# Optimization experiments

Measured on AMD Instinct MI355X. Metric: run time of the kernel, lower is better.

Reference implementation:

```python
import jax, jax.numpy as jnp
import numpy as np

C = 256
RATIO = 8
D = C // RATIO  # 32

def setup_inputs() -> dict:
    key = jax.random.key(0)
    ks = jax.random.split(key, 8)
    B, H, W = 8, 64, 64
    x = jax.random.normal(ks[0], (B, C, H, W), dtype=jnp.float32)
    s = 1.0 / np.sqrt(C)
    wq = jax.random.normal(ks[1], (D, C), dtype=jnp.float32) * s
    bq = jax.random.normal(ks[2], (D,), dtype=jnp.float32) * 0.01
    wk = jax.random.normal(ks[3], (D, C), dtype=jnp.float32) * s
    bk = jax.random.normal(ks[4], (D,), dtype=jnp.float32) * 0.01
    wv = jax.random.normal(ks[5], (C, C), dtype=jnp.float32) * s
    bv = jax.random.normal(ks[6], (C,), dtype=jnp.float32) * 0.01
    gamma = jnp.zeros((1,), dtype=jnp.float32) + 0.5  # nonzero so output depends on attention
    return {"x": x, "wq": wq, "bq": bq, "wk": wk, "bk": bk, "wv": wv, "bv": bv, "gamma": gamma}

def reference(x, wq, bq, wk, bk, wv, bv, gamma):
    B, Cc, Hh, Ww = x.shape
    N = Hh * Ww
    xf = x.reshape(B, Cc, N)                      # b c n
    q = jnp.einsum('dc,bcn->bdn', wq, xf) + bq[None, :, None]   # b d n
    k = jnp.einsum('dc,bcn->bdn', wk, xf) + bk[None, :, None]
    v = jnp.einsum('ec,bcn->ben', wv, xf) + bv[None, :, None]   # b C n
    energy = jnp.einsum('bdn,bdm->bnm', q, k)     # b n m (query n, key m)
    attn = jax.nn.softmax(energy, axis=-1)
    out = jnp.einsum('bcm,bnm->bcn', v, attn)     # out[:, :, n] = sum_m v[:, :, m]*attn[n, m]
    out = gamma[0] * out + xf
    return out.reshape(B, Cc, Hh, Ww)
```

## Files before the change

kernel.cpp:

```cpp
#include <hip/hip_runtime.h>

namespace {

using f4 = __attribute__((ext_vector_type(4))) float;
using s8 = __attribute__((ext_vector_type(8))) short;
using u16x8 = __attribute__((ext_vector_type(8))) unsigned short;

constexpr int kN = 4096;
constexpr int kC = 256;
constexpr int kD = 32;
constexpr int kB = 8;
constexpr int BR = 64;
constexpr int NT = 128;
constexpr int NI = 64;

__device__ __forceinline__ unsigned short f2bf(float x) {
  union { float f; unsigned u; } v{x};
  unsigned r = v.u + 0x7fffu + ((v.u >> 16) & 1u);
  return (unsigned short)(r >> 16);
}
__device__ __forceinline__ float bf2f(unsigned short h) {
  union { unsigned u; float f; } v{((unsigned)h) << 16};
  return v.f;
}
__device__ __forceinline__ void gll16(const void* g, void* l) {
  __builtin_amdgcn_global_load_lds(
      (const __attribute__((address_space(1))) unsigned int*)g,
      (__attribute__((address_space(3))) unsigned int*)l, 16, 0, 0);
}

__global__ void wswz_kernel(const float* __restrict__ wq,
                            const float* __restrict__ wk,
                            const float* __restrict__ wv,
                            unsigned short* __restrict__ wswz) {
  const int mt = blockIdx.x;
  const int t = threadIdx.x;
  const int s = t & 63;
  const int m = s & 15, quad = s >> 4;
  const int kk = t >> 6;
  const float* w;
  int row0;
  if (mt < 2) { w = wq; row0 = mt * 16; }
  else if (mt < 4) { w = wk; row0 = (mt - 2) * 16; }
  else { w = wv; row0 = (mt - 4) * 16; }
  const float* wrow = w + (size_t)(row0 + m) * kC;
#pragma unroll
  for (int e = 0; e < 2; ++e) {
    const int ks = kk * 2 + e;
    const int c0 = ks * 32 + quad * 8;
    u16x8 hi, lo;
#pragma unroll
    for (int j = 0; j < 8; ++j) {
      const float f = wrow[c0 + j];
      const unsigned short h = f2bf(f);
      hi[j] = h;
      lo[j] = f2bf(f - bf2f(h));
    }
    const size_t base = (size_t)mt * 8192 + (size_t)ks * 512 + (size_t)s * 8;
    *(u16x8*)&wswz[base] = hi;
    *(u16x8*)&wswz[base + 4096] = lo;
  }
}

__global__ __launch_bounds__(256, 2) void qkv_kernel(
    const float* __restrict__ x, const float* __restrict__ bq,
    const float* __restrict__ bk, const float* __restrict__ bv,
    const unsigned short* __restrict__ wswz, float* __restrict__ q,
    unsigned short* __restrict__ kswz, unsigned short* __restrict__ vswz) {
  __shared__ __align__(16) unsigned short wlds[2][8192];
  __shared__ __align__(16) unsigned short vls[16 * 72];
  const int t = threadIdx.x, lane = t & 63, wvid = t >> 6;
  const int nn = lane & 15, quad = lane >> 4;
  const int b = blockIdx.y, nb = blockIdx.x * 64;
  const int n_g = nb + wvid * 16 + nn;

  s8 xh[8], xl[8];
#pragma unroll
  for (int ks = 0; ks < 8; ++ks) {
#pragma unroll
    for (int j = 0; j < 8; ++j) {
      const int c = ks * 32 + quad * 8 + j;
      const float f = x[((size_t)(b * kC + c)) * kN + n_g];
      const unsigned short h = f2bf(f);
      xh[ks][j] = (short)h;
      xl[ks][j] = (short)f2bf(f - bf2f(h));
    }
  }

  {
    const unsigned short* gsrc = wswz;
#pragma unroll
    for (int i = 0; i < 4; ++i) {
      const int chunk = i * 4 + wvid;
      gll16(gsrc + chunk * 512 + lane * 8, &wlds[0][chunk * 512 + lane * 8]);
    }
  }

  for (int mt = 0; mt < 20; ++mt) {
    __syncthreads();
    if (mt + 1 < 20) {
      const bool nv = (mt + 1) >= 4;
      const unsigned short* gsrc = wswz + (size_t)(mt + 1) * 8192;
      unsigned short* dst = wlds[(mt + 1) & 1];
      const int niter = nv ? 2 : 4;
      for (int i = 0; i < niter; ++i) {
        const int chunk = i * 4 + wvid;
        gll16(gsrc + chunk * 512 + lane * 8, dst + chunk * 512 + lane * 8);
      }
    }
    const unsigned short* wb = wlds[mt & 1];
    const bool isv = mt >= 4;
    f4 acc = {0.f, 0.f, 0.f, 0.f};
#pragma unroll
    for (int ks = 0; ks < 8; ++ks) {
      const s8 ah = *(const s8*)&wb[ks * 512 + lane * 8];
      acc = __builtin_amdgcn_mfma_f32_16x16x32_bf16(ah, xh[ks], acc, 0, 0, 0);
      acc = __builtin_amdgcn_mfma_f32_16x16x32_bf16(ah, xl[ks], acc, 0, 0, 0);
      if (!isv) {
        const s8 al = *(const s8*)&wb[4096 + ks * 512 + lane * 8];
        acc = __builtin_amdgcn_mfma_f32_16x16x32_bf16(al, xh[ks], acc, 0, 0, 0);
      }
    }
    const int ml = quad * 4;
    if (mt < 2) {
#pragma unroll
      for (int r = 0; r < 4; ++r) {
        const float val = acc[r] + bq[mt * 16 + ml + r];
        q[((size_t)(b * kD + mt * 16 + ml + r)) * kN + n_g] = val;
      }
    } else if (mt < 4) {
      const int nt = n_g >> 5, key5 = n_g & 31;
      const int kb = key5 & 1, cpos = key5 >> 1;
      ushort4 hi, lo;
#pragma unroll
      for (int r = 0; r < 4; ++r) {
        const float val = acc[r] + bk[(mt - 2) * 16 + ml + r];
        const unsigned short h = f2bf(val);
        ((unsigned short*)&hi)[r] = h;
        ((unsigned short*)&lo)[r] = f2bf(val - bf2f(h));
      }
      const int d0 = (mt - 2) * 16 + ml;
      const int qk = d0 >> 3, j0 = d0 & 7;
      const size_t base = ((size_t)((b * NT + nt) * 4 + kb)) * 512 +
                          (size_t)(qk * 16 + cpos) * 8 + j0;
      *(ushort4*)&kswz[base] = hi;
      *(ushort4*)&kswz[base + 1024] = lo;
    } else {
      const int cb = mt - 4;
      const int tk = wvid * 16 + nn;
#pragma unroll
      for (int r = 0; r < 4; ++r) {
        const float val = acc[r] + bv[cb * 16 + ml + r];
        vls[(ml + r) * 72 + tk] = f2bf(val);
      }
      __syncthreads();
      if (t < 128) {
        const int cv = t >> 3, oct = t & 7;
        const u16x8 row = *(const u16x8*)&vls[cv * 72 + oct * 8];
        const int nt = (nb >> 5) + (oct >> 2);
        const int quadv = oct & 3;
        *(u16x8*)&vswz[((size_t)(b * NT + nt)) * 8192 + (size_t)cb * 512 +
                       (size_t)(quadv * 16 + cv) * 8] = row;
      }
    }
  }
}

__global__ __launch_bounds__(256, 2) void attn_kernel(
    const float* __restrict__ q, const unsigned short* __restrict__ kswz,
    const unsigned short* __restrict__ vswz, const float* __restrict__ x,
    const float* __restrict__ gamma, float* __restrict__ out) {
  __shared__ __align__(16) char smem[20480];
  unsigned short* const pA = (unsigned short*)smem;
  unsigned* const pAu = (unsigned*)smem;
  float* const otmp = (float*)smem;

  const int t = threadIdx.x;
  const int lane = t & 63;
  const int wvid = t >> 6;
  const int c = lane & 15;
  const int quad = lane >> 4;
  const int b = blockIdx.y;
  const int nb = blockIdx.x * BR;

  s8 qfh, qfl;
  {
    const int nq = nb + wvid * 16 + c;
#pragma unroll
    for (int j = 0; j < 8; ++j) {
      const int d = quad * 8 + j;
      const float f = q[((size_t)(b * kD + d)) * kN + nq];
      const unsigned short h = f2bf(f);
      qfh[j] = (short)h;
      qfl[j] = (short)f2bf(f - bf2f(h));
    }
  }

  s8 ones;
#pragma unroll
  for (int j = 0; j < 8; ++j) ones[j] = (short)0x3F80;

  f4 O[4][4];
#pragma unroll
  for (int i = 0; i < 4; ++i)
#pragma unroll
    for (int jj = 0; jj < 4; ++jj) O[i][jj] = (f4){0.f, 0.f, 0.f, 0.f};
  f4 Ol[4];
#pragma unroll
  for (int i = 0; i < 4; ++i) Ol[i] = (f4){0.f, 0.f, 0.f, 0.f};

  const s8* gkb = (const s8*)(kswz + ((size_t)(b * NT)) * 2048);
  const s8* gvb = (const s8*)(vswz + ((size_t)(b * NT)) * 8192);

  for (int it = 0; it < NI; ++it) {
    s8 kf[2][4], vf[2][4];
#pragma unroll
    for (int h = 0; h < 2; ++h) {
      const s8* gk = gkb + (size_t)(it * 2 + h) * 256;
#pragma unroll
      for (int f = 0; f < 4; ++f) kf[h][f] = gk[f * 64 + lane];
    }
#pragma unroll
    for (int h = 0; h < 2; ++h) {
      const s8* gv = gvb + (size_t)(it * 2 + h) * 1024;
#pragma unroll
      for (int f = 0; f < 4; ++f) vf[h][f] = gv[(wvid * 4 + f) * 64 + lane];
    }

    const f4 z = {0.f, 0.f, 0.f, 0.f};
    f4 se[2], so[2];
#pragma unroll
    for (int h = 0; h < 2; ++h) {
      f4 a = __builtin_amdgcn_mfma_f32_16x16x32_bf16(qfl, kf[h][0], z, 0, 0, 0);
      a = __builtin_amdgcn_mfma_f32_16x16x32_bf16(qfh, kf[h][2], a, 0, 0, 0);
      a = __builtin_amdgcn_mfma_f32_16x16x32_bf16(qfh, kf[h][0], a, 0, 0, 0);
      se[h] = a;
      f4 bb = __builtin_amdgcn_mfma_f32_16x16x32_bf16(qfl, kf[h][1], z, 0, 0, 0);
      bb = __builtin_amdgcn_mfma_f32_16x16x32_bf16(qfh, kf[h][3], bb, 0, 0, 0);
      bb = __builtin_amdgcn_mfma_f32_16x16x32_bf16(qfh, kf[h][1], bb, 0, 0, 0);
      so[h] = bb;
    }

#pragma unroll
    for (int h = 0; h < 2; ++h)
#pragma unroll
      for (int r = 0; r < 4; ++r) {
        const unsigned short h0 = f2bf(__expf(se[h][r]));
        const unsigned short h1 = f2bf(__expf(so[h][r]));
        pAu[(wvid * 16 + quad * 4 + r) * 36 + h * 16 + c] =
            (unsigned)h0 | ((unsigned)h1 << 16);
      }
    __syncthreads();

#pragma unroll
    for (int rb = 0; rb < 4; ++rb) {
      const s8 a0 = *(const s8*)&pA[(rb * 16 + c) * 72 + quad * 8];
      const s8 a1 = *(const s8*)&pA[(rb * 16 + c) * 72 + 32 + quad * 8];
      O[rb][0] = __builtin_amdgcn_mfma_f32_16x16x32_bf16(a0, vf[0][0], O[rb][0], 0, 0, 0);
      O[rb][1] = __builtin_amdgcn_mfma_f32_16x16x32_bf16(a0, vf[0][1], O[rb][1], 0, 0, 0);
      O[rb][2] = __builtin_amdgcn_mfma_f32_16x16x32_bf16(a0, vf[0][2], O[rb][2], 0, 0, 0);
      O[rb][3] = __builtin_amdgcn_mfma_f32_16x16x32_bf16(a0, vf[0][3], O[rb][3], 0, 0, 0);
      Ol[rb] = __builtin_amdgcn_mfma_f32_16x16x32_bf16(a0, ones, Ol[rb], 0, 0, 0);
      O[rb][0] = __builtin_amdgcn_mfma_f32_16x16x32_bf16(a1, vf[1][0], O[rb][0], 0, 0, 0);
      O[rb][1] = __builtin_amdgcn_mfma_f32_16x16x32_bf16(a1, vf[1][1], O[rb][1], 0, 0, 0);
      O[rb][2] = __builtin_amdgcn_mfma_f32_16x16x32_bf16(a1, vf[1][2], O[rb][2], 0, 0, 0);
      O[rb][3] = __builtin_amdgcn_mfma_f32_16x16x32_bf16(a1, vf[1][3], O[rb][3], 0, 0, 0);
      Ol[rb] = __builtin_amdgcn_mfma_f32_16x16x32_bf16(a1, ones, Ol[rb], 0, 0, 0);
    }
    __syncthreads();
  }

  const float gm = gamma[0];
  for (int rb = 0; rb < 4; ++rb) {
    float inv[4];
#pragma unroll
    for (int r = 0; r < 4; ++r) inv[r] = gm / Ol[rb][r];
#pragma unroll
    for (int cb = 0; cb < 4; ++cb) {
      const int ch = wvid * 64 + cb * 16 + c;
#pragma unroll
      for (int r = 0; r < 4; ++r)
        otmp[ch * 20 + quad * 4 + r] = O[rb][cb][r] * inv[r];
    }
    __syncthreads();
    {
      const int ch0 = t >> 2, rc = t & 3;
#pragma unroll
      for (int cc = 0; cc < 4; ++cc) {
        const int ch = cc * 64 + ch0;
        const f4 o4 = *(const f4*)&otmp[ch * 20 + rc * 4];
        const size_t idx =
            ((size_t)(b * kC + ch)) * kN + nb + rb * 16 + rc * 4;
        const f4 x4 = *(const f4*)&x[idx];
        *(f4*)&out[idx] = o4 + x4;
      }
    }
    __syncthreads();
  }
}

}

extern "C" void kernel_launch(void* const* d_in, const int* in_sizes, int n_in,
                              void* d_out, int out_size, void* d_ws, size_t ws_size,
                              hipStream_t stream) {
  const float* x = (const float*)d_in[0];
  const float* wq = (const float*)d_in[1];
  const float* bq = (const float*)d_in[2];
  const float* wk = (const float*)d_in[3];
  const float* bk = (const float*)d_in[4];
  const float* wv = (const float*)d_in[5];
  const float* bv = (const float*)d_in[6];
  const float* gamma = (const float*)d_in[7];
  float* out = (float*)d_out;

  float* qw = (float*)d_ws;
  unsigned short* kswz = (unsigned short*)(qw + (size_t)1048576);
  unsigned short* vswz = kswz + (size_t)2097152;
  unsigned short* wswz = vswz + (size_t)8388608;

  wswz_kernel<<<dim3(20), dim3(256), 0, stream>>>(wq, wk, wv, wswz);
  qkv_kernel<<<dim3(64, kB), dim3(256), 0, stream>>>(x, bq, bk, bv, wswz, qw,
                                                     kswz, vswz);
  attn_kernel<<<dim3(kN / BR, kB), dim3(256), 0, stream>>>(qw, kswz, vswz, x,
                                                           gamma, out);
}
```

Measured before the change: 235.7 us.

## Prefetch K/V into registers and double-buffer P in attention; drop LDS weight staging

In the attention kernel, the K/V fragments for the next key tile are now loaded into a second register set while the current tile is processed. The probability tile alternates between two LDS buffers, so each iteration needs one lgkmcnt-wait-plus-barrier instead of two __syncthreads. In the QKV kernel, the double-buffered LDS weight staging and block-wide barriers are removed: weights are read straight from global memory and each wave does its own V transpose through a private LDS slice. The cost is more register pressure from the duplicated fragment sets, and the last iteration prefetches past the end of each batch's K/V region.

```diff
diff --git a/kernel.cpp b/kernel.cpp
--- a/kernel.cpp
+++ b/kernel.cpp
@@ -23,10 +23,8 @@
   union { unsigned u; float f; } v{((unsigned)h) << 16};
   return v.f;
 }
-__device__ __forceinline__ void gll16(const void* g, void* l) {
-  __builtin_amdgcn_global_load_lds(
-      (const __attribute__((address_space(1))) unsigned int*)g,
-      (__attribute__((address_space(3))) unsigned int*)l, 16, 0, 0);
+__device__ __forceinline__ void lds_barrier() {
+  asm volatile("s_waitcnt lgkmcnt(0)\ns_barrier" ::: "memory");
 }
 
 __global__ void wswz_kernel(const float* __restrict__ wq,
@@ -67,8 +65,7 @@
     const float* __restrict__ bk, const float* __restrict__ bv,
     const unsigned short* __restrict__ wswz, float* __restrict__ q,
     unsigned short* __restrict__ kswz, unsigned short* __restrict__ vswz) {
-  __shared__ __align__(16) unsigned short wlds[2][8192];
-  __shared__ __align__(16) unsigned short vls[16 * 72];
+  __shared__ __align__(16) unsigned short vls[4][16 * 24];
   const int t = threadIdx.x, lane = t & 63, wvid = t >> 6;
   const int nn = lane & 15, quad = lane >> 4;
   const int b = blockIdx.y, nb = blockIdx.x * 64;
@@ -87,81 +84,79 @@
     }
   }
 
-  {
-    const unsigned short* gsrc = wswz;
-#pragma unroll
-    for (int i = 0; i < 4; ++i) {
-      const int chunk = i * 4 + wvid;
-      gll16(gsrc + chunk * 512 + lane * 8, &wlds[0][chunk * 512 + lane * 8]);
-    }
-  }
-
-  for (int mt = 0; mt < 20; ++mt) {
-    __syncthreads();
-    if (mt + 1 < 20) {
-      const bool nv = (mt + 1) >= 4;
-      const unsigned short* gsrc = wswz + (size_t)(mt + 1) * 8192;
-      unsigned short* dst = wlds[(mt + 1) & 1];
-      const int niter = nv ? 2 : 4;
-      for (int i = 0; i < niter; ++i) {
-        const int chunk = i * 4 + wvid;
-        gll16(gsrc + chunk * 512 + lane * 8, dst + chunk * 512 + lane * 8);
-      }
-    }
-    const unsigned short* wb = wlds[mt & 1];
-    const bool isv = mt >= 4;
-    f4 acc = {0.f, 0.f, 0.f, 0.f};
+  const s8* wf = (const s8*)wswz;
+  const f4 z = {0.f, 0.f, 0.f, 0.f};
+  const int ml = quad * 4;
+
+#pragma unroll
+  for (int mt = 0; mt < 2; ++mt) {
+    f4 acc = z;
 #pragma unroll
     for (int ks = 0; ks < 8; ++ks) {
-      const s8 ah = *(const s8*)&wb[ks * 512 + lane * 8];
+      const s8 ah = wf[mt * 1024 + ks * 64 + lane];
+      const s8 al = wf[mt * 1024 + 512 + ks * 64 + lane];
       acc = __builtin_amdgcn_mfma_f32_16x16x32_bf16(ah, xh[ks], acc, 0, 0, 0);
       acc = __builtin_amdgcn_mfma_f32_16x16x32_bf16(ah, xl[ks], acc, 0, 0, 0);
-      if (!isv) {
-        const s8 al = *(const s8*)&wb[4096 + ks * 512 + lane * 8];
-        acc = __builtin_amdgcn_mfma_f32_16x16x32_bf16(al, xh[ks], acc, 0, 0, 0);
-      }
-    }
-    const int ml = quad * 4;
-    if (mt < 2) {
-#pragma unroll
-      for (int r = 0; r < 4; ++r) {
-        const float val = acc[r] + bq[mt * 16 + ml + r];
-        q[((size_t)(b * kD + mt * 16 + ml + r)) * kN + n_g] = val;
-      }
-    } else if (mt < 4) {
-      const int nt = n_g >> 5, key5 = n_g & 31;
-      const int kb = key5 & 1, cpos = key5 >> 1;
-      ushort4 hi, lo;
-#pragma unroll
-      for (int r = 0; r < 4; ++r) {
-        const float val = acc[r] + bk[(mt - 2) * 16 + ml + r];
-        const unsigned short h = f2bf(val);
-        ((unsigned short*)&hi)[r] = h;
-        ((unsigned short*)&lo)[r] = f2bf(val - bf2f(h));
-      }
-      const int d0 = (mt - 2) * 16 + ml;
-      const int qk = d0 >> 3, j0 = d0 & 7;
-      const size_t base = ((size_t)((b * NT + nt) * 4 + kb)) * 512 +
-                          (size_t)(qk * 16 + cpos) * 8 + j0;
-      *(ushort4*)&kswz[base] = hi;
-      *(ushort4*)&kswz[base + 1024] = lo;
-    } else {
-      const int cb = mt - 4;
-      const int tk = wvid * 16 + nn;
-#pragma unroll
-      for (int r = 0; r < 4; ++r) {
-        const float val = acc[r] + bv[cb * 16 + ml + r];
-        vls[(ml + r) * 72 + tk] = f2bf(val);
-      }
-      __syncthreads();
-      if (t < 128) {
-        const int cv = t >> 3, oct = t & 7;
-        const u16x8 row = *(const u16x8*)&vls[cv * 72 + oct * 8];
-        const int nt = (nb >> 5) + (oct >> 2);
-        const int quadv = oct & 3;
-        *(u16x8*)&vswz[((size_t)(b * NT + nt)) * 8192 + (size_t)cb * 512 +
-                       (size_t)(quadv * 16 + cv) * 8] = row;
-      }
+      acc = __builtin_amdgcn_mfma_f32_16x16x32_bf16(al, xh[ks], acc, 0, 0, 0);
+    }
+#pragma unroll
+    for (int r = 0; r < 4; ++r)
+      q[((size_t)(b * kD + mt * 16 + ml + r)) * kN + n_g] =
+          acc[r] + bq[mt * 16 + ml + r];
+  }
+
+#pragma unroll
+  for (int mk = 0; mk < 2; ++mk) {
+    const int mt = 2 + mk;
+    f4 acc = z;
+#pragma unroll
+    for (int ks = 0; ks < 8; ++ks) {
+      const s8 ah = wf[mt * 1024 + ks * 64 + lane];
+      const s8 al = wf[mt * 1024 + 512 + ks * 64 + lane];
+      acc = __builtin_amdgcn_mfma_f32_16x16x32_bf16(ah, xh[ks], acc, 0, 0, 0);
+      acc = __builtin_amdgcn_mfma_f32_16x16x32_bf16(ah, xl[ks], acc, 0, 0, 0);
+      acc = __builtin_amdgcn_mfma_f32_16x16x32_bf16(al, xh[ks], acc, 0, 0, 0);
+    }
+    const int nt = n_g >> 5, key5 = n_g & 31;
+    const int kb = key5 & 1, cpos = key5 >> 1;
+    ushort4 hi, lo;
+#pragma unroll
+    for (int r = 0; r < 4; ++r) {
+      const float val = acc[r] + bk[mk * 16 + ml + r];
+      const unsigned short h = f2bf(val);
+      ((unsigned short*)&hi)[r] = h;
+      ((unsigned short*)&lo)[r] = f2bf(val - bf2f(h));
+    }
+    const int d0 = mk * 16 + ml;
+    const int qk = d0 >> 3, j0 = d0 & 7;
+    const size_t base = ((size_t)((b * NT + nt) * 4 + kb)) * 512 +
+                        (size_t)(qk * 16 + cpos) * 8 + j0;
+    *(ushort4*)&kswz[base] = hi;
+    *(ushort4*)&kswz[base + 1024] = lo;
+  }
+
+  unsigned short* vw = vls[wvid];
+  for (int cb = 0; cb < 16; ++cb) {
+    const int mt = 4 + cb;
+    f4 acc = z;
+#pragma unroll
+    for (int ks = 0; ks < 8; ++ks) {
+      const s8 ah = wf[mt * 1024 + ks * 64 + lane];
+      acc = __builtin_amdgcn_mfma_f32_16x16x32_bf16(ah, xh[ks], acc, 0, 0, 0);
+      acc = __builtin_amdgcn_mfma_f32_16x16x32_bf16(ah, xl[ks], acc, 0, 0, 0);
+    }
+#pragma unroll
+    for (int r = 0; r < 4; ++r)
+      vw[(ml + r) * 24 + nn] = f2bf(acc[r] + bv[cb * 16 + ml + r]);
+    asm volatile("s_waitcnt lgkmcnt(0)" ::: "memory");
+    if (lane < 32) {
+      const int cv = lane & 15, o = lane >> 4;
+      const u16x8 row = *(const u16x8*)&vw[cv * 24 + o * 8];
+      const int tok0 = wvid * 16 + o * 8;
+      const int nt = blockIdx.x * 2 + (tok0 >> 5);
+      const int quadv = (tok0 & 31) >> 3;
+      *(u16x8*)&vswz[((size_t)(b * NT + nt)) * 8192 + (size_t)cb * 512 +
+                     (size_t)(quadv * 16 + cv) * 8] = row;
     }
   }
 }
@@ -171,8 +166,8 @@
     const unsigned short* __restrict__ vswz, const float* __restrict__ x,
     const float* __restrict__ gamma, float* __restrict__ out) {
   __shared__ __align__(16) char smem[20480];
-  unsigned short* const pA = (unsigned short*)smem;
-  unsigned* const pAu = (unsigned*)smem;
+  unsigned* const pA0 = (unsigned*)smem;
+  unsigned* const pA1 = (unsigned*)(smem + 9216);
   float* const otmp = (float*)smem;
 
   const int t = threadIdx.x;
@@ -212,33 +207,49 @@
   const s8* gkb = (const s8*)(kswz + ((size_t)(b * NT)) * 2048);
   const s8* gvb = (const s8*)(vswz + ((size_t)(b * NT)) * 8192);
 
-  for (int it = 0; it < NI; ++it) {
-    s8 kf[2][4], vf[2][4];
-#pragma unroll
-    for (int h = 0; h < 2; ++h) {
-      const s8* gk = gkb + (size_t)(it * 2 + h) * 256;
-#pragma unroll
-      for (int f = 0; f < 4; ++f) kf[h][f] = gk[f * 64 + lane];
-    }
-#pragma unroll
-    for (int h = 0; h < 2; ++h) {
-      const s8* gv = gvb + (size_t)(it * 2 + h) * 1024;
-#pragma unroll
-      for (int f = 0; f < 4; ++f) vf[h][f] = gv[(wvid * 4 + f) * 64 + lane];
-    }
-
+  s8 kfA[2][4], vfA[2][4], kfB[2][4], vfB[2][4];
+
+#pragma unroll
+  for (int h = 0; h < 2; ++h) {
+    const s8* gk = gkb + (size_t)h * 256;
+#pragma unroll
+    for (int f = 0; f < 4; ++f) kfA[h][f] = gk[f * 64 + lane];
+  }
+#pragma unroll
+  for (int h = 0; h < 2; ++h) {
+    const s8* gv = gvb + (size_t)h * 1024;
+#pragma unroll
+    for (int f = 0; f < 4; ++f) vfA[h][f] = gv[(wvid * 4 + f) * 64 + lane];
+  }
+
+  auto iter = [&](int it, s8 (&kc)[2][4], s8 (&vc)[2][4], s8 (&kn)[2][4],
+                  s8 (&vn)[2][4], unsigned* pc) {
     const f4 z = {0.f, 0.f, 0.f, 0.f};
     f4 se[2], so[2];
 #pragma unroll
     for (int h = 0; h < 2; ++h) {
-      f4 a = __builtin_amdgcn_mfma_f32_16x16x32_bf16(qfl, kf[h][0], z, 0, 0, 0);
-      a = __builtin_amdgcn_mfma_f32_16x16x32_bf16(qfh, kf[h][2], a, 0, 0, 0);
-      a = __builtin_amdgcn_mfma_f32_16x16x32_bf16(qfh, kf[h][0], a, 0, 0, 0);
+      f4 a = __builtin_amdgcn_mfma_f32_16x16x32_bf16(qfl, kc[h][0], z, 0, 0, 0);
+      a = __builtin_amdgcn_mfma_f32_16x16x32_bf16(qfh, kc[h][2], a, 0, 0, 0);
+      a = __builtin_amdgcn_mfma_f32_16x16x32_bf16(qfh, kc[h][0], a, 0, 0, 0);
       se[h] = a;
-      f4 bb = __builtin_amdgcn_mfma_f32_16x16x32_bf16(qfl, kf[h][1], z, 0, 0, 0);
-      bb = __builtin_amdgcn_mfma_f32_16x16x32_bf16(qfh, kf[h][3], bb, 0, 0, 0);
-      bb = __builtin_amdgcn_mfma_f32_16x16x32_bf16(qfh, kf[h][1], bb, 0, 0, 0);
+      f4 bb = __builtin_amdgcn_mfma_f32_16x16x32_bf16(qfl, kc[h][1], z, 0, 0, 0);
+      bb = __builtin_amdgcn_mfma_f32_16x16x32_bf16(qfh, kc[h][3], bb, 0, 0, 0);
+      bb = __builtin_amdgcn_mfma_f32_16x16x32_bf16(qfh, kc[h][1], bb, 0, 0, 0);
       so[h] = bb;
+    }
+
+    {
+      const s8* gk = gkb + (size_t)((it + 1) * 2) * 256;
+#pragma unroll
+      for (int h = 0; h < 2; ++h)
+#pragma unroll
+        for (int f = 0; f < 4; ++f) kn[h][f] = gk[h * 256 + f * 64 + lane];
+      const s8* gv = gvb + (size_t)((it + 1) * 2) * 1024;
+#pragma unroll
+      for (int h = 0; h < 2; ++h)
+#pragma unroll
+        for (int f = 0; f < 4; ++f)
+          vn[h][f] = gv[h * 1024 + (wvid * 4 + f) * 64 + lane];
     }
 
 #pragma unroll
@@ -247,29 +258,35 @@
       for (int r = 0; r < 4; ++r) {
         const unsigned short h0 = f2bf(__expf(se[h][r]));
         const unsigned short h1 = f2bf(__expf(so[h][r]));
-        pAu[(wvid * 16 + quad * 4 + r) * 36 + h * 16 + c] =
+        pc[(wvid * 16 + quad * 4 + r) * 36 + h * 16 + c] =
             (unsigned)h0 | ((unsigned)h1 << 16);
       }
-    __syncthreads();
-
+    lds_barrier();
+
+    const unsigned short* pcs = (const unsigned short*)pc;
 #pragma unroll
     for (int rb = 0; rb < 4; ++rb) {
-      const s8 a0 = *(const s8*)&pA[(rb * 16 + c) * 72 + quad * 8];
-      const s8 a1 = *(const s8*)&pA[(rb * 16 + c) * 72 + 32 + quad * 8];
-      O[rb][0] = __builtin_amdgcn_mfma_f32_16x16x32_bf16(a0, vf[0][0], O[rb][0], 0, 0, 0);
-      O[rb][1] = __builtin_amdgcn_mfma_f32_16x16x32_bf16(a0, vf[0][1], O[rb][1], 0, 0, 0);
-      O[rb][2] = __builtin_amdgcn_mfma_f32_16x16x32_bf16(a0, vf[0][2], O[rb][2], 0, 0, 0);
-      O[rb][3] = __builtin_amdgcn_mfma_f32_16x16x32_bf16(a0, vf[0][3], O[rb][3], 0, 0, 0);
+      const s8 a0 = *(const s8*)&pcs[(rb * 16 + c) * 72 + quad * 8];
+      const s8 a1 = *(const s8*)&pcs[(rb * 16 + c) * 72 + 32 + quad * 8];
+      O[rb][0] = __builtin_amdgcn_mfma_f32_16x16x32_bf16(a0, vc[0][0], O[rb][0], 0, 0, 0);
+      O[rb][1] = __builtin_amdgcn_mfma_f32_16x16x32_bf16(a0, vc[0][1], O[rb][1], 0, 0, 0);
+      O[rb][2] = __builtin_amdgcn_mfma_f32_16x16x32_bf16(a0, vc[0][2], O[rb][2], 0, 0, 0);
+      O[rb][3] = __builtin_amdgcn_mfma_f32_16x16x32_bf16(a0, vc[0][3], O[rb][3], 0, 0, 0);
       Ol[rb] = __builtin_amdgcn_mfma_f32_16x16x32_bf16(a0, ones, Ol[rb], 0, 0, 0);
-      O[rb][0] = __builtin_amdgcn_mfma_f32_16x16x32_bf16(a1, vf[1][0], O[rb][0], 0, 0, 0);
-      O[rb][1] = __builtin_amdgcn_mfma_f32_16x16x32_bf16(a1, vf[1][1], O[rb][1], 0, 0, 0);
-      O[rb][2] = __builtin_amdgcn_mfma_f32_16x16x32_bf16(a1, vf[1][2], O[rb][2], 0, 0, 0);
-      O[rb][3] = __builtin_amdgcn_mfma_f32_16x16x32_bf16(a1, vf[1][3], O[rb][3], 0, 0, 0);
+      O[rb][0] = __builtin_amdgcn_mfma_f32_16x16x32_bf16(a1, vc[1][0], O[rb][0], 0, 0, 0);
+      O[rb][1] = __builtin_amdgcn_mfma_f32_16x16x32_bf16(a1, vc[1][1], O[rb][1], 0, 0, 0);
+      O[rb][2] = __builtin_amdgcn_mfma_f32_16x16x32_bf16(a1, vc[1][2], O[rb][2], 0, 0, 0);
+      O[rb][3] = __builtin_amdgcn_mfma_f32_16x16x32_bf16(a1, vc[1][3], O[rb][3], 0, 0, 0);
       Ol[rb] = __builtin_amdgcn_mfma_f32_16x16x32_bf16(a1, ones, Ol[rb], 0, 0, 0);
     }
-    __syncthreads();
-  }
-
+  };
+
+  for (int it2 = 0; it2 < NI / 2; ++it2) {
+    iter(2 * it2, kfA, vfA, kfB, vfB, pA0);
+    iter(2 * it2 + 1, kfB, vfB, kfA, vfA, pA1);
+  }
+
+  lds_barrier();
   const float gm = gamma[0];
   for (int rb = 0; rb < 4; ++rb) {
     float inv[4];
@@ -282,7 +299,7 @@
       for (int r = 0; r < 4; ++r)
         otmp[ch * 20 + quad * 4 + r] = O[rb][cb][r] * inv[r];
     }
-    __syncthreads();
+    lds_barrier();
     {
       const int ch0 = t >> 2, rc = t & 3;
 #pragma unroll
@@ -295,7 +312,7 @@
         *(f4*)&out[idx] = o4 + x4;
       }
     }
-    __syncthreads();
+    lds_barrier();
   }
 }
 
```

Measured after the change: 231.5 us. Within noise of the previous version (-1.8%).
